# Optimization experiments

Hardware: AMD Instinct MI355X
Metric: run time of the kernel (lower is better)

Reference implementation:

```python
import jax, jax.numpy as jnp
import numpy as np

WZ, WH, WW = 2, 6, 12          # window_size
NW = 64                        # type_of_windows = (8//2)*(96//6)
HEADS = 12
DIM = 384
B_ = 15                        # batch(1) * num_lon_windows(180//12)
N = WZ * WH * WW               # 144 tokens per window


def _construct_position_index():
    zi = np.arange(WZ); zj = -np.arange(WZ) * WZ
    hi = np.arange(WH); hj = -np.arange(WH) * WH
    w = np.arange(WW)
    c1 = np.stack(np.meshgrid(zi, hi, w, indexing='ij')).reshape(3, -1)
    c2 = np.stack(np.meshgrid(zj, hj, w, indexing='ij')).reshape(3, -1)
    coords = (c1[:, :, None] - c2[:, None, :]).transpose(1, 2, 0)  # (N, N, 3)
    coords[..., 2] += WW - 1
    coords[..., 1] *= 2 * WW - 1
    coords[..., 0] *= (2 * WW - 1) * WH * WH
    return coords.sum(-1).reshape(-1).astype(np.int32)  # (N*N,)


def setup_inputs() -> dict:
    key = jax.random.key(0)
    ks = jax.random.split(key, 6)
    bias_rows = (2 * WW - 1) * WH * WH * WZ * WZ  # 3312
    return {
        'x': jax.random.normal(ks[0], (B_, NW, N, DIM), dtype=jnp.float32),
        'mask': jnp.zeros((B_, N, N), dtype=jnp.float32),
        'w_qkv': jax.random.normal(ks[1], (DIM, 3 * DIM), dtype=jnp.float32) * 0.02,
        'b_qkv': jnp.zeros((3 * DIM,), dtype=jnp.float32),
        'w_proj': jax.random.normal(ks[2], (DIM, DIM), dtype=jnp.float32) * 0.02,
        'b_proj': jnp.zeros((DIM,), dtype=jnp.float32),
        'bias_table': jax.random.normal(ks[3], (bias_rows, NW, HEADS), dtype=jnp.float32) * 0.02,
        'position_index': jnp.asarray(_construct_position_index()),
    }


def reference(x, mask, w_qkv, b_qkv, w_proj, b_proj, bias_table, position_index):
    b_, nw, n, c = x.shape
    hd = c // HEADS
    scale = hd ** -0.5
    qkv = (x @ w_qkv + b_qkv).reshape(b_, nw, n, 3, HEADS, hd)
    q, k, v = jnp.moveaxis(qkv, 3, 0)            # each (B_, nW, N, H, hd)
    attn = jnp.einsum('bwnhd,bwmhd->bwhnm', q * scale, k)  # (B_, nW, H, N, N)
    # earth-specific relative bias gather: (N*N, nW, H) -> (nW, H, N, N)
    bias = bias_table[position_index].reshape(n, n, nw, HEADS).transpose(2, 3, 0, 1)
    attn = attn + bias[None]                     # broadcast over B_
    attn = attn + mask[:, None, None, :, :]      # additive mask per lon window
    attn = jax.nn.softmax(attn, axis=-1)         # dropout_rate=0 -> identity
    out = jnp.einsum('bwhnm,bwmhd->bwnhd', attn, v).reshape(b_, nw, n, c)
    return out @ w_proj + b_proj
```

## Files before the change

### kernel.cpp

```cpp
#include <hip/hip_runtime.h>
#include <cstdint>


typedef _Float16 f16;
typedef _Float16 f16x8 __attribute__((ext_vector_type(8)));
typedef _Float16 f16x4v __attribute__((ext_vector_type(4)));
typedef float f32x4 __attribute__((ext_vector_type(4)));

#define NW_ 64
#define HEADS_ 12
#define DIM_ 384
#define BATCH_ 15
#define NTOK_ 144
#define HD_ 32
#define MTOK_ (BATCH_*NW_*NTOK_)
#define NWH_ (BATCH_*NW_*HEADS_)

__device__ __forceinline__ void load16_lds(const void* g, void* l) {
    __builtin_amdgcn_global_load_lds(
        (const __attribute__((address_space(1))) uint32_t*)g,
        (__attribute__((address_space(3))) uint32_t*)l,
        16, 0, 0);
}

__device__ __forceinline__ f32x4 fzero4() {
    f32x4 z; z[0]=0.f; z[1]=0.f; z[2]=0.f; z[3]=0.f; return z;
}

__global__ void cvt_f32_to_f16(const float* __restrict__ src, f16* __restrict__ dst, int n4) {
    int i = blockIdx.x * blockDim.x + threadIdx.x;
    int stride = gridDim.x * blockDim.x;
    for (; i < n4; i += stride) {
        float4 v = ((const float4*)src)[i];
        f16x4v o;
        o[0] = (f16)v.x; o[1] = (f16)v.y; o[2] = (f16)v.z; o[3] = (f16)v.w;
        *(f16x4v*)(dst + 4*(size_t)i) = o;
    }
}

__global__ void transpose_cvt(const float* __restrict__ src, f16* __restrict__ dst, int K, int N) {
    int i = blockIdx.x * blockDim.x + threadIdx.x;
    if (i >= K*N) return;
    int n = i / K;
    int k = i - n*K;
    dst[i] = (f16)src[k*N + n];
}

__global__ __launch_bounds__(256) void qkv_gemm(
    const f16* __restrict__ A, const f16* __restrict__ Bt,
    const float* __restrict__ bias,
    f16* __restrict__ qws, f16* __restrict__ kws, f16* __restrict__ vws)
{
    constexpr int BK = 32;
    __shared__ __align__(16) f16 Asm[128*BK];
    __shared__ __align__(16) f16 Bsm[128*BK];
    const int tid  = threadIdx.x;
    const int lane = tid & 63;
    const int wave = tid >> 6;
    const int l15  = lane & 15;
    const int quad = lane >> 4;
    const int wr = wave >> 1, wc = wave & 1;
    const int row0 = blockIdx.x * 128;
    const int col0 = blockIdx.y * 128;

    f32x4 acc[4][4];
    #pragma unroll
    for (int i = 0; i < 4; ++i)
        #pragma unroll
        for (int j = 0; j < 4; ++j) acc[i][j] = fzero4();

    for (int kt = 0; kt < DIM_/BK; ++kt) {
        const int k0 = kt * BK;
        __syncthreads();
        #pragma unroll
        for (int cc = 0; cc < 2; ++cc) {
            int chunk  = wave*2 + cc;
            int flat16 = chunk*64 + lane;
            int r   = flat16 >> 2;
            int c16 = flat16 & 3;
            load16_lds(&A [(size_t)(row0 + r)*DIM_ + k0 + c16*8], (char*)Asm + (size_t)chunk*1024);
            load16_lds(&Bt[(size_t)(col0 + r)*DIM_ + k0 + c16*8], (char*)Bsm + (size_t)chunk*1024);
        }
        __syncthreads();

        f16x8 af[4], bf[4];
        #pragma unroll
        for (int i = 0; i < 4; ++i)
            af[i] = *(const f16x8*)&Asm[(wr*64 + i*16 + l15)*BK + quad*8];
        #pragma unroll
        for (int j = 0; j < 4; ++j)
            bf[j] = *(const f16x8*)&Bsm[(wc*64 + j*16 + l15)*BK + quad*8];
        #pragma unroll
        for (int i = 0; i < 4; ++i)
            #pragma unroll
            for (int j = 0; j < 4; ++j)
                acc[i][j] = __builtin_amdgcn_mfma_f32_16x16x32_f16(af[i], bf[j], acc[i][j], 0, 0, 0);
    }

    const int which = col0 / DIM_;
    #pragma unroll
    for (int j = 0; j < 4; ++j) {
        int col = col0 + wc*64 + j*16 + l15;
        float bq = bias[col];
        int rem = col - which*DIM_;
        int h = rem >> 5, d = rem & 31;
        #pragma unroll
        for (int i = 0; i < 4; ++i) {
            int rowb = row0 + wr*64 + i*16 + quad*4;
            #pragma unroll
            for (int r = 0; r < 4; ++r) {
                int row = rowb + r;
                int bw  = row / NTOK_;
                int n   = row - bw*NTOK_;
                int head = bw*HEADS_ + h;
                f16 hv = (f16)(acc[i][j][r] + bq);
                if (which == 0)      qws[(size_t)head*NTOK_*HD_ + n*HD_ + d] = hv;
                else if (which == 1) kws[(size_t)head*NTOK_*HD_ + n*HD_ + d] = hv;
                else                 vws[(size_t)head*HD_*NTOK_ + d*NTOK_ + n] = hv;
            }
        }
    }
}

__global__ __launch_bounds__(576) void attention(
    const f16* __restrict__ qws, const f16* __restrict__ kws, const f16* __restrict__ vws,
    const float* __restrict__ bias_table, const int* __restrict__ pos_idx,
    const float* __restrict__ mask, f16* __restrict__ ows)
{
    constexpr int KPAD = 40;
    constexpr int VPAD = 168;
    __shared__ __align__(16) char smem[10752 + 48384];
    f16* Vt  = (f16*)smem;
    f16* Ksm = (f16*)(smem + 10752);
    f16* Pst = (f16*)(smem + 10752);

    const int tid  = threadIdx.x;
    const int lane = tid & 63;
    const int wv   = tid >> 6;
    const int l15  = lane & 15;
    const int quad = lane >> 4;

    const int wh = blockIdx.x;
    const int w  = wh / HEADS_;
    const int h  = wh - w*HEADS_;

    float brg[9][4];
    #pragma unroll
    for (int j = 0; j < 9; ++j) {
        int m = j*16 + l15;
        #pragma unroll
        for (int r = 0; r < 4; ++r) {
            int n = wv*16 + quad*4 + r;
            int idx = pos_idx[n*NTOK_ + m];
            brg[j][r] = bias_table[(size_t)idx*(NW_*HEADS_) + w*HEADS_ + h];
        }
    }

    if (tid < 64) {
        int d = tid >> 1, m0 = 144 + (tid & 1)*8;
        uint4 z = {0u,0u,0u,0u};
        *(uint4*)&Vt[d*VPAD + m0] = z;
    }

    const float scale = 0.17677669529663687f;

    for (int b = 0; b < BATCH_; ++b) {
        const int bwh = (b*NW_ + w)*HEADS_ + h;
        const f16* qh = qws + (size_t)bwh*NTOK_*HD_;
        const f16* kh = kws + (size_t)bwh*NTOK_*HD_;
        const f16* vh = vws + (size_t)bwh*HD_*NTOK_;

        __syncthreads();
        {
            int flat = tid*8;
            int n = flat >> 5, d = flat & 31;
            *(uint4*)&Ksm[n*KPAD + d] = *(const uint4*)&kh[flat];
            int dv = flat / NTOK_;
            int mv = flat - dv*NTOK_;
            *(uint4*)&Vt[dv*VPAD + mv] = *(const uint4*)&vh[flat];
        }
        int nq = wv*16 + l15;
        f16x8 qf = *(const f16x8*)&qh[nq*HD_ + quad*8];
        __syncthreads();

        f32x4 sfr[9];
        #pragma unroll
        for (int j = 0; j < 9; ++j) {
            f16x8 kf = *(const f16x8*)&Ksm[(j*16 + l15)*KPAD + quad*8];
            sfr[j] = __builtin_amdgcn_mfma_f32_16x16x32_f16(qf, kf, fzero4(), 0, 0, 0);
        }
        __syncthreads();

        float p[9][4], rmax[4], rsum[4];
        #pragma unroll
        for (int r = 0; r < 4; ++r) rmax[r] = -1e30f;
        const float* mrow = mask + (size_t)b*NTOK_*NTOK_;
        #pragma unroll
        for (int j = 0; j < 9; ++j) {
            int m = j*16 + l15;
            #pragma unroll
            for (int r = 0; r < 4; ++r) {
                int n = wv*16 + quad*4 + r;
                float s = sfr[j][r]*scale + brg[j][r] + mrow[n*NTOK_ + m];
                p[j][r] = s;
                rmax[r] = fmaxf(rmax[r], s);
            }
        }
        #pragma unroll
        for (int r = 0; r < 4; ++r) {
            float v = rmax[r];
            #pragma unroll
            for (int off = 1; off < 16; off <<= 1)
                v = fmaxf(v, __shfl_xor(v, off, 64));
            rmax[r] = v;
        }
        #pragma unroll
        for (int r = 0; r < 4; ++r) rsum[r] = 0.f;
        #pragma unroll
        for (int j = 0; j < 9; ++j)
            #pragma unroll
            for (int r = 0; r < 4; ++r) {
                float e = __expf(p[j][r] - rmax[r]);
                p[j][r] = e;
                rsum[r] += e;
            }
        #pragma unroll
        for (int r = 0; r < 4; ++r) {
            float v = rsum[r];
            #pragma unroll
            for (int off = 1; off < 16; off <<= 1)
                v += __shfl_xor(v, off, 64);
            rsum[r] = 1.0f / v;
        }

        f16* Pw = Pst + wv*16*VPAD;
        #pragma unroll
        for (int j = 0; j < 9; ++j) {
            int m = j*16 + l15;
            #pragma unroll
            for (int r = 0; r < 4; ++r)
                Pw[(quad*4 + r)*VPAD + m] = (f16)(p[j][r]*rsum[r]);
        }
        if (lane < 32) {
            int row = lane >> 1, m0 = 144 + (lane & 1)*8;
            uint4 z = {0u,0u,0u,0u};
            *(uint4*)&Pw[row*VPAD + m0] = z;
        }

        f32x4 o0 = fzero4(), o1 = fzero4();
        #pragma unroll
        for (int s = 0; s < 5; ++s) {
            f16x8 pa = *(const f16x8*)&Pw[l15*VPAD + s*32 + quad*8];
            f16x8 v0 = *(const f16x8*)&Vt[l15*VPAD + s*32 + quad*8];
            f16x8 v1 = *(const f16x8*)&Vt[(16 + l15)*VPAD + s*32 + quad*8];
            o0 = __builtin_amdgcn_mfma_f32_16x16x32_f16(pa, v0, o0, 0, 0, 0);
            o1 = __builtin_amdgcn_mfma_f32_16x16x32_f16(pa, v1, o1, 0, 0, 0);
        }

        const int bw = b*NW_ + w;
        #pragma unroll
        for (int r = 0; r < 4; ++r) {
            int n = wv*16 + quad*4 + r;
            size_t base = ((size_t)bw*NTOK_ + n)*DIM_ + h*HD_;
            ows[base + l15]      = (f16)o0[r];
            ows[base + 16 + l15] = (f16)o1[r];
        }
    }
}

__global__ __launch_bounds__(256) void proj_gemm(
    const f16* __restrict__ A, const f16* __restrict__ Bt,
    const float* __restrict__ bias, float* __restrict__ out)
{
    constexpr int BK = 32;
    __shared__ __align__(16) f16 Asm[128*BK];
    __shared__ __align__(16) f16 Bsm[128*BK];
    const int tid  = threadIdx.x;
    const int lane = tid & 63;
    const int wave = tid >> 6;
    const int l15  = lane & 15;
    const int quad = lane >> 4;
    const int wr = wave >> 1, wc = wave & 1;
    const int row0 = blockIdx.x * 128;
    const int col0 = blockIdx.y * 128;

    f32x4 acc[4][4];
    #pragma unroll
    for (int i = 0; i < 4; ++i)
        #pragma unroll
        for (int j = 0; j < 4; ++j) acc[i][j] = fzero4();

    for (int kt = 0; kt < DIM_/BK; ++kt) {
        const int k0 = kt * BK;
        __syncthreads();
        #pragma unroll
        for (int cc = 0; cc < 2; ++cc) {
            int chunk  = wave*2 + cc;
            int flat16 = chunk*64 + lane;
            int r   = flat16 >> 2;
            int c16 = flat16 & 3;
            load16_lds(&A [(size_t)(row0 + r)*DIM_ + k0 + c16*8], (char*)Asm + (size_t)chunk*1024);
            load16_lds(&Bt[(size_t)(col0 + r)*DIM_ + k0 + c16*8], (char*)Bsm + (size_t)chunk*1024);
        }
        __syncthreads();

        f16x8 af[4], bf[4];
        #pragma unroll
        for (int i = 0; i < 4; ++i)
            af[i] = *(const f16x8*)&Asm[(wr*64 + i*16 + l15)*BK + quad*8];
        #pragma unroll
        for (int j = 0; j < 4; ++j)
            bf[j] = *(const f16x8*)&Bsm[(wc*64 + j*16 + l15)*BK + quad*8];
        #pragma unroll
        for (int i = 0; i < 4; ++i)
            #pragma unroll
            for (int j = 0; j < 4; ++j)
                acc[i][j] = __builtin_amdgcn_mfma_f32_16x16x32_f16(af[i], bf[j], acc[i][j], 0, 0, 0);
    }

    #pragma unroll
    for (int j = 0; j < 4; ++j) {
        int col = col0 + wc*64 + j*16 + l15;
        float bp = bias[col];
        #pragma unroll
        for (int i = 0; i < 4; ++i) {
            int rowb = row0 + wr*64 + i*16 + quad*4;
            #pragma unroll
            for (int r = 0; r < 4; ++r)
                out[(size_t)(rowb + r)*DIM_ + col] = acc[i][j][r] + bp;
        }
    }
}

extern "C" void kernel_launch(void* const* d_in, const int* in_sizes, int n_in,
                              void* d_out, int out_size, void* d_ws, size_t ws_size,
                              hipStream_t stream)
{
    const float* x      = (const float*)d_in[0];
    const float* mask   = (const float*)d_in[1];
    const float* w_qkv  = (const float*)d_in[2];
    const float* b_qkv  = (const float*)d_in[3];
    const float* w_proj = (const float*)d_in[4];
    const float* b_proj = (const float*)d_in[5];
    const float* btab   = (const float*)d_in[6];
    const int*   pidx   = (const int*)d_in[7];
    float* out = (float*)d_out;

    constexpr size_t X16_B = (size_t)MTOK_*DIM_*2;
    constexpr size_t WTQ_B = (size_t)1152*384*2;
    constexpr size_t WTP_B = (size_t)384*384*2;
    constexpr size_t HEAD_B = (size_t)NWH_*NTOK_*HD_*2;

    char* ws = (char*)d_ws;
    f16* x16 = (f16*)ws;
    f16* wtq = (f16*)(ws + X16_B);
    f16* wtp = (f16*)(ws + X16_B + WTQ_B);
    f16* qws = (f16*)(ws + X16_B + WTQ_B + WTP_B);
    f16* kws = (f16*)((char*)qws + HEAD_B);
    f16* vws = (f16*)((char*)kws + HEAD_B);
    f16* ows = x16;

    cvt_f32_to_f16<<<8192, 256, 0, stream>>>(x, x16, MTOK_*DIM_/4);
    transpose_cvt<<<(384*1152 + 255)/256, 256, 0, stream>>>(w_qkv, wtq, 384, 1152);
    transpose_cvt<<<(384*384  + 255)/256, 256, 0, stream>>>(w_proj, wtp, 384, 384);
    qkv_gemm<<<dim3(MTOK_/128, 1152/128), 256, 0, stream>>>(x16, wtq, b_qkv, qws, kws, vws);
    attention<<<NW_*HEADS_, 576, 0, stream>>>(qws, kws, vws, btab, pidx, mask, ows);
    proj_gemm<<<dim3(MTOK_/128, DIM_/128), 256, 0, stream>>>(ows, wtp, b_proj, out);
}
```

Baseline: 1.070 ms.

## Double-buffer LDS in QKV and projection GEMMs and remap blocks across XCDs

Both GEMM kernels now keep two LDS stages, so the global-to-LDS load of the next K tile is issued before the MFMA work on the current tile, with one barrier per iteration instead of two. The 2D grid is flattened to 1D and remapped so that consecutive hardware block IDs, which are spread round-robin over the 8 XCDs, land on neighbouring tiles within the same XCD for better L2 reuse. This doubles LDS use per block, which may reduce occupancy, and the remap hardcodes the grid sizes (9720 and 3240 blocks).

```diff
diff --git a/kernel.cpp b/kernel.cpp
--- a/kernel.cpp
+++ b/kernel.cpp
@@ -52,16 +52,20 @@
     f16* __restrict__ qws, f16* __restrict__ kws, f16* __restrict__ vws)
 {
     constexpr int BK = 32;
-    __shared__ __align__(16) f16 Asm[128*BK];
-    __shared__ __align__(16) f16 Bsm[128*BK];
+    constexpr int NT = DIM_/BK;
+    __shared__ __align__(16) f16 Asm[2][128*BK];
+    __shared__ __align__(16) f16 Bsm[2][128*BK];
     const int tid  = threadIdx.x;
     const int lane = tid & 63;
     const int wave = tid >> 6;
     const int l15  = lane & 15;
     const int quad = lane >> 4;
     const int wr = wave >> 1, wc = wave & 1;
-    const int row0 = blockIdx.x * 128;
-    const int col0 = blockIdx.y * 128;
+
+    unsigned lin = blockIdx.x;
+    lin = (lin & 7u) * 1215u + (lin >> 3);
+    const int row0 = (int)(lin / 9u) * 128;
+    const int col0 = (int)(lin % 9u) * 128;
 
     f32x4 acc[4][4];
     #pragma unroll
@@ -69,33 +73,47 @@
         #pragma unroll
         for (int j = 0; j < 4; ++j) acc[i][j] = fzero4();
 
-    for (int kt = 0; kt < DIM_/BK; ++kt) {
+    auto stage = [&](int kt, int b) {
         const int k0 = kt * BK;
-        __syncthreads();
         #pragma unroll
         for (int cc = 0; cc < 2; ++cc) {
             int chunk  = wave*2 + cc;
             int flat16 = chunk*64 + lane;
             int r   = flat16 >> 2;
             int c16 = flat16 & 3;
-            load16_lds(&A [(size_t)(row0 + r)*DIM_ + k0 + c16*8], (char*)Asm + (size_t)chunk*1024);
-            load16_lds(&Bt[(size_t)(col0 + r)*DIM_ + k0 + c16*8], (char*)Bsm + (size_t)chunk*1024);
-        }
-        __syncthreads();
-
+            load16_lds(&A [(size_t)(row0 + r)*DIM_ + k0 + c16*8], (char*)(&Asm[b][0]) + chunk*1024);
+            load16_lds(&Bt[(size_t)(col0 + r)*DIM_ + k0 + c16*8], (char*)(&Bsm[b][0]) + chunk*1024);
+        }
+    };
+    auto compute = [&](int b) {
         f16x8 af[4], bf[4];
         #pragma unroll
         for (int i = 0; i < 4; ++i)
-            af[i] = *(const f16x8*)&Asm[(wr*64 + i*16 + l15)*BK + quad*8];
+            af[i] = *(const f16x8*)&Asm[b][(wr*64 + i*16 + l15)*BK + quad*8];
         #pragma unroll
         for (int j = 0; j < 4; ++j)
-            bf[j] = *(const f16x8*)&Bsm[(wc*64 + j*16 + l15)*BK + quad*8];
+            bf[j] = *(const f16x8*)&Bsm[b][(wc*64 + j*16 + l15)*BK + quad*8];
         #pragma unroll
         for (int i = 0; i < 4; ++i)
             #pragma unroll
             for (int j = 0; j < 4; ++j)
                 acc[i][j] = __builtin_amdgcn_mfma_f32_16x16x32_f16(af[i], bf[j], acc[i][j], 0, 0, 0);
-    }
+    };
+
+    stage(0, 0);
+    asm volatile("s_waitcnt vmcnt(0)" ::: "memory");
+    __builtin_amdgcn_s_barrier();
+    __builtin_amdgcn_sched_barrier(0);
+    int cur = 0;
+    for (int kt = 0; kt < NT-1; ++kt) {
+        stage(kt+1, cur^1);
+        compute(cur);
+        asm volatile("s_waitcnt vmcnt(0) lgkmcnt(0)" ::: "memory");
+        __builtin_amdgcn_s_barrier();
+        __builtin_amdgcn_sched_barrier(0);
+        cur ^= 1;
+    }
+    compute(cur);
 
     const int which = col0 / DIM_;
     #pragma unroll
@@ -273,16 +291,20 @@
     const float* __restrict__ bias, float* __restrict__ out)
 {
     constexpr int BK = 32;
-    __shared__ __align__(16) f16 Asm[128*BK];
-    __shared__ __align__(16) f16 Bsm[128*BK];
+    constexpr int NT = DIM_/BK;
+    __shared__ __align__(16) f16 Asm[2][128*BK];
+    __shared__ __align__(16) f16 Bsm[2][128*BK];
     const int tid  = threadIdx.x;
     const int lane = tid & 63;
     const int wave = tid >> 6;
     const int l15  = lane & 15;
     const int quad = lane >> 4;
     const int wr = wave >> 1, wc = wave & 1;
-    const int row0 = blockIdx.x * 128;
-    const int col0 = blockIdx.y * 128;
+
+    unsigned lin = blockIdx.x;
+    lin = (lin & 7u) * 405u + (lin >> 3);
+    const int row0 = (int)(lin / 3u) * 128;
+    const int col0 = (int)(lin % 3u) * 128;
 
     f32x4 acc[4][4];
     #pragma unroll
@@ -290,33 +312,47 @@
         #pragma unroll
         for (int j = 0; j < 4; ++j) acc[i][j] = fzero4();
 
-    for (int kt = 0; kt < DIM_/BK; ++kt) {
+    auto stage = [&](int kt, int b) {
         const int k0 = kt * BK;
-        __syncthreads();
         #pragma unroll
         for (int cc = 0; cc < 2; ++cc) {
             int chunk  = wave*2 + cc;
             int flat16 = chunk*64 + lane;
             int r   = flat16 >> 2;
             int c16 = flat16 & 3;
-            load16_lds(&A [(size_t)(row0 + r)*DIM_ + k0 + c16*8], (char*)Asm + (size_t)chunk*1024);
-            load16_lds(&Bt[(size_t)(col0 + r)*DIM_ + k0 + c16*8], (char*)Bsm + (size_t)chunk*1024);
-        }
-        __syncthreads();
-
+            load16_lds(&A [(size_t)(row0 + r)*DIM_ + k0 + c16*8], (char*)(&Asm[b][0]) + chunk*1024);
+            load16_lds(&Bt[(size_t)(col0 + r)*DIM_ + k0 + c16*8], (char*)(&Bsm[b][0]) + chunk*1024);
+        }
+    };
+    auto compute = [&](int b) {
         f16x8 af[4], bf[4];
         #pragma unroll
         for (int i = 0; i < 4; ++i)
-            af[i] = *(const f16x8*)&Asm[(wr*64 + i*16 + l15)*BK + quad*8];
+            af[i] = *(const f16x8*)&Asm[b][(wr*64 + i*16 + l15)*BK + quad*8];
         #pragma unroll
         for (int j = 0; j < 4; ++j)
-            bf[j] = *(const f16x8*)&Bsm[(wc*64 + j*16 + l15)*BK + quad*8];
+            bf[j] = *(const f16x8*)&Bsm[b][(wc*64 + j*16 + l15)*BK + quad*8];
         #pragma unroll
         for (int i = 0; i < 4; ++i)
             #pragma unroll
             for (int j = 0; j < 4; ++j)
                 acc[i][j] = __builtin_amdgcn_mfma_f32_16x16x32_f16(af[i], bf[j], acc[i][j], 0, 0, 0);
-    }
+    };
+
+    stage(0, 0);
+    asm volatile("s_waitcnt vmcnt(0)" ::: "memory");
+    __builtin_amdgcn_s_barrier();
+    __builtin_amdgcn_sched_barrier(0);
+    int cur = 0;
+    for (int kt = 0; kt < NT-1; ++kt) {
+        stage(kt+1, cur^1);
+        compute(cur);
+        asm volatile("s_waitcnt vmcnt(0) lgkmcnt(0)" ::: "memory");
+        __builtin_amdgcn_s_barrier();
+        __builtin_amdgcn_sched_barrier(0);
+        cur ^= 1;
+    }
+    compute(cur);
 
     #pragma unroll
     for (int j = 0; j < 4; ++j) {
@@ -363,7 +399,7 @@
     cvt_f32_to_f16<<<8192, 256, 0, stream>>>(x, x16, MTOK_*DIM_/4);
     transpose_cvt<<<(384*1152 + 255)/256, 256, 0, stream>>>(w_qkv, wtq, 384, 1152);
     transpose_cvt<<<(384*384  + 255)/256, 256, 0, stream>>>(w_proj, wtp, 384, 384);
-    qkv_gemm<<<dim3(MTOK_/128, 1152/128), 256, 0, stream>>>(x16, wtq, b_qkv, qws, kws, vws);
+    qkv_gemm<<<9720, 256, 0, stream>>>(x16, wtq, b_qkv, qws, kws, vws);
     attention<<<NW_*HEADS_, 576, 0, stream>>>(qws, kws, vws, btab, pidx, mask, ows);
-    proj_gemm<<<dim3(MTOK_/128, DIM_/128), 256, 0, stream>>>(ows, wtp, b_proj, out);
-}
+    proj_gemm<<<3240, 256, 0, stream>>>(ows, wtp, b_proj, out);
+}
```

New measurement: 1.035 ms. 3.3% less time.
